# Optimization experiments

Hardware: AMD Instinct MI355X
Metric: run time of the kernel (lower is better)

The kernel has to match this reference:

```python
import jax, jax.numpy as jnp
import numpy as np

B, N = 128, 1369
DINO, CLIP, H = 384, 512, 8
D = CLIP // H  # head_dim = 64
EPS = 1e-5


def setup_inputs() -> dict:
    key = jax.random.key(0)
    ks = jax.random.split(key, 8)
    s_clip = 1.0 / np.sqrt(CLIP)
    s_dino = 1.0 / np.sqrt(DINO)
    return {
        "dino_features": jax.random.normal(ks[0], (B, N, DINO), jnp.float32),
        "clip_features": jax.random.normal(ks[1], (B, CLIP), jnp.float32),
        "Wq": jax.random.uniform(ks[2], (CLIP, CLIP), jnp.float32, -s_clip, s_clip),
        "bq": jnp.zeros((CLIP,), jnp.float32),
        "Wk": jax.random.uniform(ks[3], (DINO, CLIP), jnp.float32, -s_dino, s_dino),
        "bk": jnp.zeros((CLIP,), jnp.float32),
        "Wv": jax.random.uniform(ks[4], (DINO, CLIP), jnp.float32, -s_dino, s_dino),
        "bv": jnp.zeros((CLIP,), jnp.float32),
        "temperature": jnp.ones((1,), jnp.float32),
        "ln_gamma": jnp.ones((CLIP,), jnp.float32),
        "ln_beta": jnp.zeros((CLIP,), jnp.float32),
    }


def reference(dino_features, clip_features, Wq, bq, Wk, bk, Wv, bv,
              temperature, ln_gamma, ln_beta):
    # Q: (B, H, D) -- single query token from CLIP
    Q = (clip_features @ Wq + bq).reshape(B, H, D)
    # K, V: (B, N, H, D)
    K = (dino_features @ Wk + bk).reshape(B, N, H, D)
    V = (dino_features @ Wv + bv).reshape(B, N, H, D)
    scale = jnp.sqrt(jnp.float32(D)) * temperature[0]
    # attention logits over patches: (B, H, N)
    logits = jnp.einsum("bhd,bnhd->bhn", Q, K) / scale
    attn = jax.nn.softmax(logits, axis=-1)  # dropout is identity in eval mode
    out = jnp.einsum("bhn,bnhd->bhd", attn, V).reshape(B, CLIP)
    # LayerNorm over last dim
    mu = out.mean(axis=-1, keepdims=True)
    var = out.var(axis=-1, keepdims=True)
    return (out - mu) * jax.lax.rsqrt(var + EPS) * ln_gamma + ln_beta
```

## Files before the change

### kernel.cpp

```cpp
#include <hip/hip_runtime.h>
#include <math.h>
#include <stdint.h>

#define B_    128
#define N_    1369
#define DINO_ 384
#define CLIP_ 512
#define H_    8
#define CHUNKS 6
#define CH     229
#define TROWS  8
#define DEPTH  4
#define SEGW   3
#define SMP    52

__device__ __forceinline__ float wave_sum(float v) {
  v += __shfl_xor(v, 1);  v += __shfl_xor(v, 2);  v += __shfl_xor(v, 4);
  v += __shfl_xor(v, 8);  v += __shfl_xor(v, 16); v += __shfl_xor(v, 32);
  return v;
}

__device__ __forceinline__ void gld16(const float* g, float* lds_base) {
  __builtin_amdgcn_global_load_lds(
      (const __attribute__((address_space(1))) void*)g,
      (__attribute__((address_space(3))) void*)lds_base, 16, 0, 0);
}

__global__ __launch_bounds__(256) void kq(const float* __restrict__ clip,
                                          const float* __restrict__ Wq,
                                          const float* __restrict__ bq,
                                          float* __restrict__ Q) {
  const int b = blockIdx.x;
  const int c = blockIdx.y * 256 + threadIdx.x;
  __shared__ float cl[CLIP_];
  cl[threadIdx.x] = clip[b * CLIP_ + threadIdx.x];
  cl[threadIdx.x + 256] = clip[b * CLIP_ + threadIdx.x + 256];
  __syncthreads();
  float acc = bq[c];
  #pragma unroll 8
  for (int j = 0; j < CLIP_; ++j) acc += cl[j] * Wq[j * CLIP_ + c];
  Q[b * CLIP_ + c] = acc;
}

__global__ __launch_bounds__(256) void kqk(const float* __restrict__ Wk,
                                           const float* __restrict__ Q,
                                           const float* __restrict__ temp,
                                           float* __restrict__ qkout) {
  const int b = blockIdx.x;
  const int e = blockIdx.y * 256 + threadIdx.x;
  __shared__ float qs[CLIP_];
  qs[threadIdx.x] = Q[b * CLIP_ + threadIdx.x];
  qs[threadIdx.x + 256] = Q[b * CLIP_ + threadIdx.x + 256];
  __syncthreads();
  const int h = e / DINO_;
  const int j = e - h * DINO_;
  const float rs = 1.0f / (8.0f * temp[0]);
  const float* wrow = Wk + (size_t)j * CLIP_ + h * 64;
  const float* qrow = qs + h * 64;
  float a0 = 0.f, a1 = 0.f, a2 = 0.f, a3 = 0.f;
  #pragma unroll
  for (int d = 0; d < 64; d += 4) {
    const float4 wv = *(const float4*)(wrow + d);
    const float4 qv = *(const float4*)(qrow + d);
    a0 += wv.x * qv.x;  a1 += wv.y * qv.y;
    a2 += wv.z * qv.z;  a3 += wv.w * qv.w;
  }
  qkout[(size_t)b * 3072 + e] = ((a0 + a1) + (a2 + a3)) * rs;
}

__global__ __launch_bounds__(256, 3) void kmain(const float* __restrict__ dino,
                                                const float* __restrict__ qk,
                                                float* __restrict__ ps,
                                                float* __restrict__ pl) {
  __shared__ float lds[DEPTH * TROWS * DINO_];
  __shared__ float lm[2][H_];

  const int blk = blockIdx.x;
  const int b = blk / CHUNKS;
  const int c = blk - b * CHUNKS;
  const int n0 = c * CH;
  const int n1 = min(N_, n0 + CH);
  const int tid = threadIdx.x, w = tid >> 6, lane = tid & 63;
  const int m = lane & 31;
  const int G = lane >> 5;
  const int b4 = (lane >> 4) & 1, b3 = (lane >> 3) & 1;
  const int hO = 2 * b4 + b3;

  float qr[4][12];
  {
    const float* qb = qk + (size_t)b * 3072 + (G * 4) * DINO_ + 4 * m;
    #pragma unroll
    for (int j = 0; j < 4; ++j)
      #pragma unroll
      for (int t = 0; t < 3; ++t) {
        const float4 v = *(const float4*)(qb + j * DINO_ + 128 * t);
        qr[j][4*t] = v.x; qr[j][4*t+1] = v.y; qr[j][4*t+2] = v.z; qr[j][4*t+3] = v.w;
      }
  }
  asm volatile("s_waitcnt vmcnt(0)" ::: "memory");

  float s[4][12];
  #pragma unroll
  for (int j = 0; j < 4; ++j)
    #pragma unroll
    for (int q = 0; q < 12; ++q) s[j][q] = 0.0f;
  float l = 0.0f;

  const float* gdino = dino + (size_t)b * N_ * DINO_;
  const float* gclamp = dino + ((size_t)B_ * N_ * DINO_ - 4);
  const int ntiles = (n1 - n0 + TROWS - 1) / TROWS;

  #pragma unroll
  for (int pt = 0; pt < 3; ++pt) {
    const float* gb = gdino + (size_t)(n0 + pt * TROWS) * DINO_;
    float* buf = lds + pt * (TROWS * DINO_);
    #pragma unroll
    for (int j = 0; j < SEGW; ++j) {
      const int sg = SEGW * w + j;
      const float* g = gb + sg * 256 + 4 * lane;
      if (g > gclamp) g = gclamp;
      gld16(g, buf + sg * 256);
    }
  }

  for (int t = 0; t < ntiles; ++t) {
    asm volatile("s_waitcnt vmcnt(6)" ::: "memory");
    __builtin_amdgcn_sched_barrier(0);
    {
      const float* gb = gdino + (size_t)(n0 + (t + 3) * TROWS) * DINO_;
      float* buf = lds + ((t + 3) & 3) * (TROWS * DINO_);
      #pragma unroll
      for (int j = 0; j < SEGW; ++j) {
        const int sg = SEGW * w + j;
        const float* g = gb + sg * 256 + 4 * lane;
        if (g > gclamp) g = gclamp;
        gld16(g, buf + sg * 256);
      }
    }
    const float* cur = lds + (t & 3) * (TROWS * DINO_);
    const int tb = n0 + t * TROWS;
    #pragma unroll
    for (int k = 0; k < 2; ++k) {
      const int slot = 2 * w + k;
      if (tb + slot < n1) {
        const float* xr = cur + slot * DINO_ + 4 * m;
        const float4 x0 = *(const float4*)(xr);
        const float4 x1 = *(const float4*)(xr + 128);
        const float4 x2 = *(const float4*)(xr + 256);
        const float xv[12] = {x0.x, x0.y, x0.z, x0.w,
                              x1.x, x1.y, x1.z, x1.w,
                              x2.x, x2.y, x2.z, x2.w};
        float va[4];
        #pragma unroll
        for (int j = 0; j < 4; ++j) {
          float a = 0.f, bacc = 0.f;
          #pragma unroll
          for (int q = 0; q < 12; q += 2) {
            a    += qr[j][q]     * xv[q];
            bacc += qr[j][q + 1] * xv[q + 1];
          }
          va[j] = a + bacc;
        }
        float c0, c1;
        {
          const float t0 = __shfl_xor(va[0], 16), t1 = __shfl_xor(va[1], 16);
          const float t2 = __shfl_xor(va[2], 16), t3 = __shfl_xor(va[3], 16);
          c0 = b4 ? va[2] + t2 : va[0] + t0;
          c1 = b4 ? va[3] + t3 : va[1] + t1;
        }
        float d;
        {
          const float u0 = __shfl_xor(c0, 8), u1 = __shfl_xor(c1, 8);
          d = b3 ? c1 + u1 : c0 + u0;
        }
        d += __shfl_xor(d, 4);
        d += __shfl_xor(d, 2);
        d += __shfl_xor(d, 1);
        const float p = __expf(d);
        l += p;
        float P[4];
        P[0] = p;
        P[1] = __shfl_xor(p, 8);
        P[2] = __shfl_xor(p, 16);
        P[3] = __shfl_xor(P[1], 16);
        #pragma unroll
        for (int j = 0; j < 4; ++j)
          #pragma unroll
          for (int q = 0; q < 12; ++q) s[j][q] += P[j] * xv[q];
      }
    }
  }

  asm volatile("s_waitcnt vmcnt(0)" ::: "memory");
  __syncthreads();

  float* sm0 = lds;
  float* sm1 = lds + 64 * SMP;
  if (w >= 2) {
    float* dst = (w == 2 ? sm0 : sm1) + lane * SMP;
    #pragma unroll
    for (int j = 0; j < 4; ++j)
      #pragma unroll
      for (int t = 0; t < 3; ++t)
        *(float4*)(dst + j * 12 + 4 * t) =
            make_float4(s[j][4*t], s[j][4*t+1], s[j][4*t+2], s[j][4*t+3]);
    if ((lane & 7) == 0) lm[w - 2][4 * G + hO] = l;
  }
  __syncthreads();
  if (w < 2) {
    const float* src = (w == 0 ? sm0 : sm1) + lane * SMP;
    #pragma unroll
    for (int j = 0; j < 4; ++j)
      #pragma unroll
      for (int t = 0; t < 3; ++t) {
        const float4 v = *(const float4*)(src + j * 12 + 4 * t);
        s[j][4*t] += v.x; s[j][4*t+1] += v.y; s[j][4*t+2] += v.z; s[j][4*t+3] += v.w;
      }
    l += lm[w][4 * G + hO];
  }
  __syncthreads();
  if (w == 1) {
    float* dst = sm0 + lane * SMP;
    #pragma unroll
    for (int j = 0; j < 4; ++j)
      #pragma unroll
      for (int t = 0; t < 3; ++t)
        *(float4*)(dst + j * 12 + 4 * t) =
            make_float4(s[j][4*t], s[j][4*t+1], s[j][4*t+2], s[j][4*t+3]);
    if ((lane & 7) == 0) lm[0][4 * G + hO] = l;
  }
  __syncthreads();
  if (w == 0) {
    const float* src = sm0 + lane * SMP;
    #pragma unroll
    for (int j = 0; j < 4; ++j)
      #pragma unroll
      for (int t = 0; t < 3; ++t) {
        const float4 v = *(const float4*)(src + j * 12 + 4 * t);
        s[j][4*t] += v.x; s[j][4*t+1] += v.y; s[j][4*t+2] += v.z; s[j][4*t+3] += v.w;
      }
    l += lm[0][4 * G + hO];
    float* pso = ps + (size_t)blk * 3072;
    #pragma unroll
    for (int j = 0; j < 4; ++j) {
      const int h = 4 * G + (hO ^ j);
      float* o = pso + h * DINO_ + 4 * m;
      #pragma unroll
      for (int t = 0; t < 3; ++t)
        *(float4*)(o + 128 * t) =
            make_float4(s[j][4*t], s[j][4*t+1], s[j][4*t+2], s[j][4*t+3]);
    }
    if ((lane & 7) == 0) pl[blk * H_ + 4 * G + hO] = l;
  }
}

__global__ __launch_bounds__(512) void kmf(const float* __restrict__ ps,
                                           const float* __restrict__ pl,
                                           const float* __restrict__ Wv,
                                           const float* __restrict__ bv,
                                           const float* __restrict__ gamma,
                                           const float* __restrict__ beta,
                                           float* __restrict__ out) {
  const int b = blockIdx.x, tid = threadIdx.x;
  __shared__ float sfl[3072];
  __shared__ float rL[H_];
  float a[6];
  #pragma unroll
  for (int r = 0; r < 6; ++r) {
    const int e = tid + 512 * r;
    float acc = 0.0f;
    #pragma unroll
    for (int cc = 0; cc < CHUNKS; ++cc)
      acc += ps[(size_t)(b * CHUNKS + cc) * 3072 + e];
    a[r] = acc;
  }
  if (tid < H_) {
    float L = 0.0f;
    #pragma unroll
    for (int cc = 0; cc < CHUNKS; ++cc) L += pl[(b * CHUNKS + cc) * H_ + tid];
    rL[tid] = 1.0f / L;
  }
  __syncthreads();
  #pragma unroll
  for (int r = 0; r < 6; ++r) {
    const int e = tid + 512 * r;
    sfl[e] = a[r] * rL[e / DINO_];
  }
  __syncthreads();
  const int w = tid >> 6, lane = tid & 63;
  const float* srow = sfl + (tid >> 6) * DINO_;
  float acc = bv[tid];
  #pragma unroll 8
  for (int d = 0; d < DINO_; ++d) acc += srow[d] * Wv[d * CLIP_ + tid];
  float sum = wave_sum(acc);
  float sq  = wave_sum(acc * acc);
  __shared__ float rS[8], rQ[8];
  if (lane == 0) { rS[w] = sum; rQ[w] = sq; }
  __syncthreads();
  float tot = 0.0f, totq = 0.0f;
  #pragma unroll
  for (int i = 0; i < 8; ++i) { tot += rS[i]; totq += rQ[i]; }
  const float mu = tot * (1.0f / 512.0f);
  const float var = totq * (1.0f / 512.0f) - mu * mu;
  const float rstd = rsqrtf(var + 1e-5f);
  out[(size_t)b * CLIP_ + tid] = (acc - mu) * rstd * gamma[tid] + beta[tid];
}

extern "C" void kernel_launch(void* const* d_in, const int* in_sizes, int n_in,
                              void* d_out, int out_size, void* d_ws, size_t ws_size,
                              hipStream_t stream) {
  const float* dino  = (const float*)d_in[0];
  const float* clip  = (const float*)d_in[1];
  const float* Wq    = (const float*)d_in[2];
  const float* bq    = (const float*)d_in[3];
  const float* Wk    = (const float*)d_in[4];
  const float* Wv    = (const float*)d_in[6];
  const float* bv    = (const float*)d_in[7];
  const float* temp  = (const float*)d_in[8];
  const float* gamma = (const float*)d_in[9];
  const float* beta  = (const float*)d_in[10];
  float* out = (float*)d_out;

  float* ws  = (float*)d_ws;
  float* Q   = ws;
  float* qkb = Q   + 65536;
  float* ps  = qkb + 393216;
  float* pl  = ps  + 2359296;

  kq   <<<dim3(B_, 2),  256, 0, stream>>>(clip, Wq, bq, Q);
  kqk  <<<dim3(B_, 12), 256, 0, stream>>>(Wk, Q, temp, qkb);
  kmain<<<B_ * CHUNKS,  256, 0, stream>>>(dino, qkb, ps, pl);
  kmf  <<<B_,           512, 0, stream>>>(ps, pl, Wv, bv, gamma, beta, out);
}
```

Measured before the change: 470.6 us.

## Remap kmain lanes to 16-lane head groups with DPP reductions

Restructures the per-wave work mapping in the attention kernel. Each 16-lane group now owns two heads over a 24-element slice, instead of 32-lane groups owning four heads over 12 elements. The cross-lane shuffle/select cascade for the logits and the probability broadcast is replaced by a 4-step DPP row reduction. The invalid-row branch becomes predication, and the sched_barrier is removed. Every lane now does the same FMA count while the shuffle traffic drops, but register pressure rises with 96 live floats against the 256,3 launch bounds, so spilling is a risk.

After: 466.2 us. About the same (-0.9%).

```diff
diff --git a/kernel.cpp b/kernel.cpp
--- a/kernel.cpp
+++ b/kernel.cpp
@@ -20,6 +20,18 @@
   return v;
 }
 
+__device__ __forceinline__ float sum16_dpp(float v) {
+  v += __int_as_float(__builtin_amdgcn_update_dpp(
+      0, __float_as_int(v), 0x121, 0xf, 0xf, false));
+  v += __int_as_float(__builtin_amdgcn_update_dpp(
+      0, __float_as_int(v), 0x122, 0xf, 0xf, false));
+  v += __int_as_float(__builtin_amdgcn_update_dpp(
+      0, __float_as_int(v), 0x124, 0xf, 0xf, false));
+  v += __int_as_float(__builtin_amdgcn_update_dpp(
+      0, __float_as_int(v), 0x128, 0xf, 0xf, false));
+  return v;
+}
+
 __device__ __forceinline__ void gld16(const float* g, float* lds_base) {
   __builtin_amdgcn_global_load_lds(
       (const __attribute__((address_space(1))) void*)g,
@@ -81,30 +93,27 @@
   const int n0 = c * CH;
   const int n1 = min(N_, n0 + CH);
   const int tid = threadIdx.x, w = tid >> 6, lane = tid & 63;
-  const int m = lane & 31;
-  const int G = lane >> 5;
-  const int b4 = (lane >> 4) & 1, b3 = (lane >> 3) & 1;
-  const int hO = 2 * b4 + b3;
-
-  float qr[4][12];
+  const int r = lane >> 4;
+  const int m = lane & 15;
+  const int off = 4 * m;
+
+  float qr0[24], qr1[24];
   {
-    const float* qb = qk + (size_t)b * 3072 + (G * 4) * DINO_ + 4 * m;
-    #pragma unroll
-    for (int j = 0; j < 4; ++j)
-      #pragma unroll
-      for (int t = 0; t < 3; ++t) {
-        const float4 v = *(const float4*)(qb + j * DINO_ + 128 * t);
-        qr[j][4*t] = v.x; qr[j][4*t+1] = v.y; qr[j][4*t+2] = v.z; qr[j][4*t+3] = v.w;
-      }
+    const float* qb = qk + (size_t)b * 3072 + off;
+    #pragma unroll
+    for (int t = 0; t < 6; ++t) {
+      const float4 v0 = *(const float4*)(qb + r * DINO_ + 64 * t);
+      const float4 v1 = *(const float4*)(qb + (r + 4) * DINO_ + 64 * t);
+      qr0[4*t] = v0.x; qr0[4*t+1] = v0.y; qr0[4*t+2] = v0.z; qr0[4*t+3] = v0.w;
+      qr1[4*t] = v1.x; qr1[4*t+1] = v1.y; qr1[4*t+2] = v1.z; qr1[4*t+3] = v1.w;
+    }
   }
   asm volatile("s_waitcnt vmcnt(0)" ::: "memory");
 
-  float s[4][12];
-  #pragma unroll
-  for (int j = 0; j < 4; ++j)
-    #pragma unroll
-    for (int q = 0; q < 12; ++q) s[j][q] = 0.0f;
-  float l = 0.0f;
+  float s0[24], s1[24];
+  #pragma unroll
+  for (int q = 0; q < 24; ++q) { s0[q] = 0.0f; s1[q] = 0.0f; }
+  float l0 = 0.0f, l1 = 0.0f;
 
   const float* gdino = dino + (size_t)b * N_ * DINO_;
   const float* gclamp = dino + ((size_t)B_ * N_ * DINO_ - 4);
@@ -125,7 +134,6 @@
 
   for (int t = 0; t < ntiles; ++t) {
     asm volatile("s_waitcnt vmcnt(6)" ::: "memory");
-    __builtin_amdgcn_sched_barrier(0);
     {
       const float* gb = gdino + (size_t)(n0 + (t + 3) * TROWS) * DINO_;
       float* buf = lds + ((t + 3) & 3) * (TROWS * DINO_);
@@ -142,51 +150,32 @@
     #pragma unroll
     for (int k = 0; k < 2; ++k) {
       const int slot = 2 * w + k;
-      if (tb + slot < n1) {
-        const float* xr = cur + slot * DINO_ + 4 * m;
-        const float4 x0 = *(const float4*)(xr);
-        const float4 x1 = *(const float4*)(xr + 128);
-        const float4 x2 = *(const float4*)(xr + 256);
-        const float xv[12] = {x0.x, x0.y, x0.z, x0.w,
-                              x1.x, x1.y, x1.z, x1.w,
-                              x2.x, x2.y, x2.z, x2.w};
-        float va[4];
-        #pragma unroll
-        for (int j = 0; j < 4; ++j) {
-          float a = 0.f, bacc = 0.f;
-          #pragma unroll
-          for (int q = 0; q < 12; q += 2) {
-            a    += qr[j][q]     * xv[q];
-            bacc += qr[j][q + 1] * xv[q + 1];
-          }
-          va[j] = a + bacc;
-        }
-        float c0, c1;
-        {
-          const float t0 = __shfl_xor(va[0], 16), t1 = __shfl_xor(va[1], 16);
-          const float t2 = __shfl_xor(va[2], 16), t3 = __shfl_xor(va[3], 16);
-          c0 = b4 ? va[2] + t2 : va[0] + t0;
-          c1 = b4 ? va[3] + t3 : va[1] + t1;
-        }
-        float d;
-        {
-          const float u0 = __shfl_xor(c0, 8), u1 = __shfl_xor(c1, 8);
-          d = b3 ? c1 + u1 : c0 + u0;
-        }
-        d += __shfl_xor(d, 4);
-        d += __shfl_xor(d, 2);
-        d += __shfl_xor(d, 1);
-        const float p = __expf(d);
-        l += p;
-        float P[4];
-        P[0] = p;
-        P[1] = __shfl_xor(p, 8);
-        P[2] = __shfl_xor(p, 16);
-        P[3] = __shfl_xor(P[1], 16);
-        #pragma unroll
-        for (int j = 0; j < 4; ++j)
-          #pragma unroll
-          for (int q = 0; q < 12; ++q) s[j][q] += P[j] * xv[q];
+      const bool valid = (tb + slot) < n1;
+      const float* xr = cur + slot * DINO_ + off;
+      float xv[24];
+      #pragma unroll
+      for (int t6 = 0; t6 < 6; ++t6) {
+        const float4 xx = *(const float4*)(xr + 64 * t6);
+        xv[4*t6] = xx.x; xv[4*t6+1] = xx.y; xv[4*t6+2] = xx.z; xv[4*t6+3] = xx.w;
+      }
+      float a0 = 0.f, a1 = 0.f, b0 = 0.f, b1 = 0.f;
+      #pragma unroll
+      for (int q = 0; q < 24; q += 2) {
+        a0 += qr0[q]     * xv[q];
+        a1 += qr0[q + 1] * xv[q + 1];
+        b0 += qr1[q]     * xv[q];
+        b1 += qr1[q + 1] * xv[q + 1];
+      }
+      float va0 = sum16_dpp(a0 + a1);
+      float va1 = sum16_dpp(b0 + b1);
+      const float p0 = valid ? __expf(va0) : 0.0f;
+      const float p1 = valid ? __expf(va1) : 0.0f;
+      l0 += p0;
+      l1 += p1;
+      #pragma unroll
+      for (int q = 0; q < 24; ++q) {
+        s0[q] += p0 * xv[q];
+        s1[q] += p1 * xv[q];
       }
     }
   }
@@ -199,58 +188,56 @@
   if (w >= 2) {
     float* dst = (w == 2 ? sm0 : sm1) + lane * SMP;
     #pragma unroll
-    for (int j = 0; j < 4; ++j)
-      #pragma unroll
-      for (int t = 0; t < 3; ++t)
-        *(float4*)(dst + j * 12 + 4 * t) =
-            make_float4(s[j][4*t], s[j][4*t+1], s[j][4*t+2], s[j][4*t+3]);
-    if ((lane & 7) == 0) lm[w - 2][4 * G + hO] = l;
+    for (int t = 0; t < 6; ++t) {
+      *(float4*)(dst + 4 * t)      = make_float4(s0[4*t], s0[4*t+1], s0[4*t+2], s0[4*t+3]);
+      *(float4*)(dst + 24 + 4 * t) = make_float4(s1[4*t], s1[4*t+1], s1[4*t+2], s1[4*t+3]);
+    }
+    if (m == 0) { lm[w - 2][r] = l0; lm[w - 2][r + 4] = l1; }
   }
   __syncthreads();
   if (w < 2) {
     const float* src = (w == 0 ? sm0 : sm1) + lane * SMP;
     #pragma unroll
-    for (int j = 0; j < 4; ++j)
-      #pragma unroll
-      for (int t = 0; t < 3; ++t) {
-        const float4 v = *(const float4*)(src + j * 12 + 4 * t);
-        s[j][4*t] += v.x; s[j][4*t+1] += v.y; s[j][4*t+2] += v.z; s[j][4*t+3] += v.w;
-      }
-    l += lm[w][4 * G + hO];
+    for (int t = 0; t < 6; ++t) {
+      const float4 v0 = *(const float4*)(src + 4 * t);
+      const float4 v1 = *(const float4*)(src + 24 + 4 * t);
+      s0[4*t] += v0.x; s0[4*t+1] += v0.y; s0[4*t+2] += v0.z; s0[4*t+3] += v0.w;
+      s1[4*t] += v1.x; s1[4*t+1] += v1.y; s1[4*t+2] += v1.z; s1[4*t+3] += v1.w;
+    }
+    l0 += lm[w][r];
+    l1 += lm[w][r + 4];
   }
   __syncthreads();
   if (w == 1) {
     float* dst = sm0 + lane * SMP;
     #pragma unroll
-    for (int j = 0; j < 4; ++j)
-      #pragma unroll
-      for (int t = 0; t < 3; ++t)
-        *(float4*)(dst + j * 12 + 4 * t) =
-            make_float4(s[j][4*t], s[j][4*t+1], s[j][4*t+2], s[j][4*t+3]);
-    if ((lane & 7) == 0) lm[0][4 * G + hO] = l;
+    for (int t = 0; t < 6; ++t) {
+      *(float4*)(dst + 4 * t)      = make_float4(s0[4*t], s0[4*t+1], s0[4*t+2], s0[4*t+3]);
+      *(float4*)(dst + 24 + 4 * t) = make_float4(s1[4*t], s1[4*t+1], s1[4*t+2], s1[4*t+3]);
+    }
+    if (m == 0) { lm[0][r] = l0; lm[0][r + 4] = l1; }
   }
   __syncthreads();
   if (w == 0) {
     const float* src = sm0 + lane * SMP;
     #pragma unroll
-    for (int j = 0; j < 4; ++j)
-      #pragma unroll
-      for (int t = 0; t < 3; ++t) {
-        const float4 v = *(const float4*)(src + j * 12 + 4 * t);
-        s[j][4*t] += v.x; s[j][4*t+1] += v.y; s[j][4*t+2] += v.z; s[j][4*t+3] += v.w;
-      }
-    l += lm[0][4 * G + hO];
+    for (int t = 0; t < 6; ++t) {
+      const float4 v0 = *(const float4*)(src + 4 * t);
+      const float4 v1 = *(const float4*)(src + 24 + 4 * t);
+      s0[4*t] += v0.x; s0[4*t+1] += v0.y; s0[4*t+2] += v0.z; s0[4*t+3] += v0.w;
+      s1[4*t] += v1.x; s1[4*t+1] += v1.y; s1[4*t+2] += v1.z; s1[4*t+3] += v1.w;
+    }
+    l0 += lm[0][r];
+    l1 += lm[0][r + 4];
     float* pso = ps + (size_t)blk * 3072;
     #pragma unroll
-    for (int j = 0; j < 4; ++j) {
-      const int h = 4 * G + (hO ^ j);
-      float* o = pso + h * DINO_ + 4 * m;
-      #pragma unroll
-      for (int t = 0; t < 3; ++t)
-        *(float4*)(o + 128 * t) =
-            make_float4(s[j][4*t], s[j][4*t+1], s[j][4*t+2], s[j][4*t+3]);
-    }
-    if ((lane & 7) == 0) pl[blk * H_ + 4 * G + hO] = l;
+    for (int t = 0; t < 6; ++t) {
+      *(float4*)(pso + r * DINO_ + 64 * t + off) =
+          make_float4(s0[4*t], s0[4*t+1], s0[4*t+2], s0[4*t+3]);
+      *(float4*)(pso + (r + 4) * DINO_ + 64 * t + off) =
+          make_float4(s1[4*t], s1[4*t+1], s1[4*t+2], s1[4*t+3]);
+    }
+    if (m == 0) { pl[blk * H_ + r] = l0; pl[blk * H_ + r + 4] = l1; }
   }
 }
 
```
